# Kernel optimization log

Measured on AMD Instinct MI355X. Metric: run time of the kernel, lower is better.

The kernel has to match this reference:

```python
import jax, jax.numpy as jnp
import numpy as np

N = 8192          # number of atoms
N_ELEM = 95       # r2r4 table size (elements 0..94)
EPS = 1e-12


def setup_inputs() -> dict:
    key = jax.random.key(0)
    k1, k2, k3 = jax.random.split(key, 3)
    atomic_numbers = jax.random.randint(k1, (N,), 0, N_ELEM)
    # positions in a ~60 Angstrom box so pair distances are realistic
    positions = jax.random.uniform(k2, (N, 3), dtype=jnp.float32) * 60.0
    r2r4 = jax.random.uniform(k3, (N_ELEM,), dtype=jnp.float32)
    # Becke-Johnson damping parameters (PBE D3-BJ)
    a1 = jnp.float32(0.4289)
    a2 = jnp.float32(4.4407)
    s6 = jnp.float32(1.0)
    s8 = jnp.float32(0.7875)
    return {"atomic_numbers": atomic_numbers, "positions": positions,
            "r2r4": r2r4, "a1": a1, "a2": a2, "s6": s6, "s8": s8}


def reference(atomic_numbers, positions, r2r4, a1, a2, s6, s8):
    # Per-atom-type gather (present in source; mathematically unused because
    # the source hard-codes c6 = c8 = 1 via all-ones LazyTensors).
    r2r4_z = r2r4[atomic_numbers]                      # (N,)

    # All-pairs squared distances. d appears only as d^6 and d^8, which are
    # polynomials in d2, so no sqrt is needed (also keeps diagonal smooth).
    diff = positions[:, None, :] - positions[None, :, :]   # (N, N, 3)
    d2 = jnp.sum(diff * diff, axis=-1)                     # (N, N)
    d6 = d2 * d2 * d2
    d8 = d6 * d2

    # c6 = c8 = 1  =>  tmp = a1 * sqrt(c8/c6) + a2 = a1 + a2
    tmp = a1 + a2
    tmp2 = tmp * tmp
    tmp6 = tmp2 * tmp2 * tmp2
    tmp8 = tmp6 * tmp2

    c6 = jnp.float32(1.0)
    c8 = jnp.float32(1.0)
    D_ij = -s6 * c6 / (d6 + tmp6 + EPS) - s8 * c8 / (d8 + tmp8 + EPS)

    # mask d > eps  <=>  d2 > eps^2 (removes self-terms)
    mask = d2 > EPS * EPS
    D_ij = jnp.where(mask, D_ij, jnp.float32(0.0))

    # a_i = sum_j D_ij ; energy = sum_i a_i
    return jnp.sum(D_ij) + jnp.float32(0.0) * jnp.sum(r2r4_z)
```

## Files before the change

### kernel.cpp

```cpp
#include <hip/hip_runtime.h>

#define NA 8192
#define IT 128
#define JT 64
#define NI (NA / IT)
#define NJOB 4160
#define NBODY (NJOB * JT)
#define NWAVE 4096
#define BPW 65
#define WPB 8
#define BLOCK (WPB * 64)
#define NBLK (NWAVE / WPB)
#define S_OF(I) ((I) * (129 - (I)))

typedef float v2f __attribute__((ext_vector_type(2)));
typedef float v4f __attribute__((ext_vector_type(4)));

__global__ __launch_bounds__(BLOCK, 4) void dftd3_pair_energy(
    const float* __restrict__ pos,
    const float* __restrict__ p_a1, const float* __restrict__ p_a2,
    const float* __restrict__ p_s6, const float* __restrict__ p_s8,
    float* __restrict__ partial, int* __restrict__ cnt,
    float* __restrict__ out)
{
    const int tid  = threadIdx.x;
    const int lane = tid & 63;
    const int wv   = tid >> 6;
    const int q = __builtin_amdgcn_readfirstlane(blockIdx.x * WPB + wv);

    __shared__ v4f jtile[WPB][JT];
    __shared__ float wsum[WPB];
    __shared__ int lastflag;

    const float a1 = p_a1[0], a2 = p_a2[0];
    const float s6 = p_s6[0], s8 = p_s8[0];
    const float tmp  = a1 + a2;
    const float tmp2 = tmp * tmp;
    const float tmp6 = tmp2 * tmp2 * tmp2;
    const float tmp8 = tmp6 * tmp2;
    const float T6 = tmp6 + 1e-12f;
    const float T8 = tmp8 + 1e-12f;
    const float SC  = 3.5527137e-15f;
    const float ns6 = -s6 * SC;
    const float ns8 = -s8 * SC;

    const int b0   = q * BPW;
    const int jobA = b0 >> 6;
    const int kA   = b0 & 63;

    int I = (int)((129.0f - sqrtf(16641.0f - 4.0f * (float)jobA)) * 0.5f);
    if (I < 0) I = 0;
    if (I > NI - 1) I = NI - 1;
    while (S_OF(I + 1) <= jobA) ++I;
    while (S_OF(I) > jobA) --I;
    int J = 2 * I + (jobA - S_OF(I));

    v2f xi, yi, zi;
    int i0 = 0;
    int Jbase = 0;

    auto load_i = [&](int It) {
        i0 = It * IT + 2 * lane;
        xi = (v2f){ pos[3 * i0 + 0], pos[3 * i0 + 3] };
        yi = (v2f){ pos[3 * i0 + 1], pos[3 * i0 + 4] };
        zi = (v2f){ pos[3 * i0 + 2], pos[3 * i0 + 5] };
    };
    auto stage_j = [&](int Jt) {
        int j = Jt * JT + lane;
        jtile[wv][lane] = (v4f){ pos[3 * j + 0], pos[3 * j + 1], pos[3 * j + 2], 0.0f };
    };

    v2f acc = {0.0f, 0.0f};

    auto body = [&](int k, bool masked) {
        v4f pj = jtile[wv][k];
        v2f dx = xi - pj.x;
        v2f dy = yi - pj.y;
        v2f dz = zi - pj.z;
        v2f d2 = __builtin_elementwise_fma(dx, dx,
                 __builtin_elementwise_fma(dy, dy, dz * dz));
        v2f d4 = d2 * d2;
        v2f A  = __builtin_elementwise_fma(d4, d2, (v2f)T6);
        v2f B  = __builtin_elementwise_fma(d4, d4, (v2f)T8);
        v2f num = __builtin_elementwise_fma((v2f)ns6, B, (v2f)ns8 * A);
        v2f den = A * B;
        v2f dens = den * (v2f)SC;
        float t = dens.x * dens.y;
        float r = __builtin_amdgcn_rcpf(t);
        if (masked) {
            int jk = Jbase + k;
            num.x = (jk > i0)     ? num.x : 0.0f;
            num.y = (jk > i0 + 1) ? num.y : 0.0f;
        }
        v2f rec = __builtin_shufflevector(dens, dens, 1, 0) * r;
        acc = __builtin_elementwise_fma(num, rec, acc);
    };

    auto run = [&](int k0, int k1, bool edge) {
        if (edge) {
            #pragma unroll 8
            for (int k = k0; k < k1; ++k) body(k, true);
        } else {
            #pragma unroll 8
            for (int k = k0; k < k1; ++k) body(k, false);
        }
    };

    load_i(I);
    stage_j(J);
    Jbase = J * JT;
    run(kA, JT, (J - 2 * I) < 2);

    int I2 = I, J2 = J + 1;
    if (J == 127) { I2 = I + 1; J2 = 2 * I2; }
    if (I2 != I) load_i(I2);
    stage_j(J2);
    Jbase = J2 * JT;
    run(0, kA + 1, (J2 - 2 * I2) < 2);

    float accs = 2.0f * (acc.x + acc.y);

    #pragma unroll
    for (int off = 32; off > 0; off >>= 1)
        accs += __shfl_xor(accs, off, 64);

    if (lane == 0) wsum[wv] = accs;
    __syncthreads();
    if (tid == 0) {
        float s = 0.0f;
        #pragma unroll
        for (int p = 0; p < WPB; ++p) s += wsum[p];
        atomicExch(&partial[blockIdx.x], s);
        __threadfence();
        int old = atomicAdd(cnt, 1);
        lastflag = (old == NBLK - 1);
    }
    __syncthreads();
    if (lastflag) {
        __threadfence();
        float s = 0.0f;
        for (int tt = tid; tt < NBLK; tt += BLOCK)
            s += atomicAdd(&partial[tt], 0.0f);
        #pragma unroll
        for (int off = 32; off > 0; off >>= 1)
            s += __shfl_xor(s, off, 64);
        if (lane == 0) wsum[wv] = s;
        __syncthreads();
        if (tid == 0) {
            float tot = 0.0f;
            #pragma unroll
            for (int p = 0; p < WPB; ++p) tot += wsum[p];
            out[0] = tot;
        }
    }
}

extern "C" void kernel_launch(void* const* d_in, const int* in_sizes, int n_in,
                              void* d_out, int out_size, void* d_ws, size_t ws_size,
                              hipStream_t stream) {
    const float* pos = (const float*)d_in[1];
    const float* a1  = (const float*)d_in[3];
    const float* a2  = (const float*)d_in[4];
    const float* s6  = (const float*)d_in[5];
    const float* s8  = (const float*)d_in[6];
    float* partial = (float*)d_ws;
    int*   cnt     = (int*)((char*)d_ws + 65536);
    float* out     = (float*)d_out;

    hipMemsetAsync(cnt, 0, sizeof(int), stream);

    dftd3_pair_energy<<<dim3(NBLK), BLOCK, 0, stream>>>(pos, a1, a2, s6, s8,
                                                        partial, cnt, out);
}
```

Baseline: 84.60 us.

## Expand pair distance algebraically and replace atomic-counter reduction with cooperative grid sync

Pair distances are now computed as |ri|^2+|rj|^2-2ri·rj using positions pre-scaled by a power of two, with the squared norm stored in the fourth slot of the shared j-tile. This saves a subtraction per component in the inner loop, and the scaling constants are folded into T6/T8 and the numerators instead of a separate SC multiply. The final reduction drops the memset and last-block counter in favour of a cooperative launch with a grid-wide sync, after which block 0 sums the partials. The expanded distance form risks cancellation error for nearby atoms, and the grid sync requires all 512 blocks to be co-resident.

```diff
diff --git a/kernel.cpp b/kernel.cpp
--- a/kernel.cpp
+++ b/kernel.cpp
@@ -1,4 +1,5 @@
 #include <hip/hip_runtime.h>
+#include <hip/hip_cooperative_groups.h>
 
 #define NA 8192
 #define IT 128
@@ -16,11 +17,13 @@
 typedef float v2f __attribute__((ext_vector_type(2)));
 typedef float v4f __attribute__((ext_vector_type(4)));
 
+namespace cg = cooperative_groups;
+
 __global__ __launch_bounds__(BLOCK, 4) void dftd3_pair_energy(
     const float* __restrict__ pos,
     const float* __restrict__ p_a1, const float* __restrict__ p_a2,
     const float* __restrict__ p_s6, const float* __restrict__ p_s8,
-    float* __restrict__ partial, int* __restrict__ cnt,
+    float* __restrict__ partial,
     float* __restrict__ out)
 {
     const int tid  = threadIdx.x;
@@ -30,7 +33,6 @@
 
     __shared__ v4f jtile[WPB][JT];
     __shared__ float wsum[WPB];
-    __shared__ int lastflag;
 
     const float a1 = p_a1[0], a2 = p_a2[0];
     const float s6 = p_s6[0], s8 = p_s8[0];
@@ -38,11 +40,13 @@
     const float tmp2 = tmp * tmp;
     const float tmp6 = tmp2 * tmp2 * tmp2;
     const float tmp8 = tmp6 * tmp2;
-    const float T6 = tmp6 + 1e-12f;
-    const float T8 = tmp8 + 1e-12f;
-    const float SC  = 3.5527137e-15f;
-    const float ns6 = -s6 * SC;
-    const float ns8 = -s8 * SC;
+    const float H  = 0.0625f;
+    const float C3 = 5.9604645e-8f;
+    const float C4 = 2.3283064365386963e-10f;
+    const float T6 = (tmp6 + 1e-12f) * C3;
+    const float T8 = (tmp8 + 1e-12f) * C4;
+    const float ns6 = -s6 * C3;
+    const float ns8 = -s8 * C4;
 
     const int b0   = q * BPW;
     const int jobA = b0 >> 6;
@@ -55,44 +59,51 @@
     while (S_OF(I) > jobA) --I;
     int J = 2 * I + (jobA - S_OF(I));
 
-    v2f xi, yi, zi;
+    v2f xim, yim, zim, peri2;
     int i0 = 0;
     int Jbase = 0;
 
     auto load_i = [&](int It) {
         i0 = It * IT + 2 * lane;
-        xi = (v2f){ pos[3 * i0 + 0], pos[3 * i0 + 3] };
-        yi = (v2f){ pos[3 * i0 + 1], pos[3 * i0 + 4] };
-        zi = (v2f){ pos[3 * i0 + 2], pos[3 * i0 + 5] };
+        v2f xr = { pos[3 * i0 + 0], pos[3 * i0 + 3] };
+        v2f yr = { pos[3 * i0 + 1], pos[3 * i0 + 4] };
+        v2f zr = { pos[3 * i0 + 2], pos[3 * i0 + 5] };
+        v2f xs = xr * (v2f)H, ys = yr * (v2f)H, zs = zr * (v2f)H;
+        peri2 = __builtin_elementwise_fma(xs, xs,
+                __builtin_elementwise_fma(ys, ys, zs * zs));
+        xim = xs * (v2f)-2.0f;
+        yim = ys * (v2f)-2.0f;
+        zim = zs * (v2f)-2.0f;
     };
     auto stage_j = [&](int Jt) {
         int j = Jt * JT + lane;
-        jtile[wv][lane] = (v4f){ pos[3 * j + 0], pos[3 * j + 1], pos[3 * j + 2], 0.0f };
+        float xj = pos[3 * j + 0] * H;
+        float yj = pos[3 * j + 1] * H;
+        float zj = pos[3 * j + 2] * H;
+        float wj = fmaf(xj, xj, fmaf(yj, yj, zj * zj));
+        jtile[wv][lane] = (v4f){ xj, yj, zj, wj };
     };
 
     v2f acc = {0.0f, 0.0f};
 
     auto body = [&](int k, bool masked) {
         v4f pj = jtile[wv][k];
-        v2f dx = xi - pj.x;
-        v2f dy = yi - pj.y;
-        v2f dz = zi - pj.z;
-        v2f d2 = __builtin_elementwise_fma(dx, dx,
-                 __builtin_elementwise_fma(dy, dy, dz * dz));
+        v2f d2 = __builtin_elementwise_fma(xim, (v2f)pj.x,
+                 __builtin_elementwise_fma(yim, (v2f)pj.y,
+                 __builtin_elementwise_fma(zim, (v2f)pj.z, peri2 + pj.w)));
         v2f d4 = d2 * d2;
         v2f A  = __builtin_elementwise_fma(d4, d2, (v2f)T6);
         v2f B  = __builtin_elementwise_fma(d4, d4, (v2f)T8);
         v2f num = __builtin_elementwise_fma((v2f)ns6, B, (v2f)ns8 * A);
         v2f den = A * B;
-        v2f dens = den * (v2f)SC;
-        float t = dens.x * dens.y;
+        float t = den.x * den.y;
         float r = __builtin_amdgcn_rcpf(t);
         if (masked) {
             int jk = Jbase + k;
             num.x = (jk > i0)     ? num.x : 0.0f;
             num.y = (jk > i0 + 1) ? num.y : 0.0f;
         }
-        v2f rec = __builtin_shufflevector(dens, dens, 1, 0) * r;
+        v2f rec = __builtin_shufflevector(den, den, 1, 0) * r;
         acc = __builtin_elementwise_fma(num, rec, acc);
     };
 
@@ -132,15 +143,12 @@
         for (int p = 0; p < WPB; ++p) s += wsum[p];
         atomicExch(&partial[blockIdx.x], s);
         __threadfence();
-        int old = atomicAdd(cnt, 1);
-        lastflag = (old == NBLK - 1);
     }
-    __syncthreads();
-    if (lastflag) {
-        __threadfence();
-        float s = 0.0f;
-        for (int tt = tid; tt < NBLK; tt += BLOCK)
-            s += atomicAdd(&partial[tt], 0.0f);
+
+    cg::this_grid().sync();
+
+    if (blockIdx.x == 0) {
+        float s = atomicAdd(&partial[tid], 0.0f);
         #pragma unroll
         for (int off = 32; off > 0; off >>= 1)
             s += __shfl_xor(s, off, 64);
@@ -164,11 +172,10 @@
     const float* s6  = (const float*)d_in[5];
     const float* s8  = (const float*)d_in[6];
     float* partial = (float*)d_ws;
-    int*   cnt     = (int*)((char*)d_ws + 65536);
     float* out     = (float*)d_out;
 
-    hipMemsetAsync(cnt, 0, sizeof(int), stream);
-
-    dftd3_pair_energy<<<dim3(NBLK), BLOCK, 0, stream>>>(pos, a1, a2, s6, s8,
-                                                        partial, cnt, out);
+    void* args[] = { (void*)&pos, (void*)&a1, (void*)&a2, (void*)&s6, (void*)&s8,
+                     (void*)&partial, (void*)&out };
+    hipLaunchCooperativeKernel(reinterpret_cast<void*>(dftd3_pair_energy),
+                               dim3(NBLK), dim3(BLOCK), args, 0, stream);
 }
```

After: 139.3 us. +64.7%, slower.
